# Optimization experiments

Measured on AMD Instinct MI355X. Metric: run time of the kernel, lower is better.

The kernel has to match this reference:

```python
import jax, jax.numpy as jnp
import numpy as np

EPS = 1e-5  # norm_eps


def setup_inputs() -> dict:
    key = jax.random.key(0)
    ks = jax.random.split(key, 9)
    N, C, T, H, W = 2, 1024, 8, 28, 28
    Di = 512
    s = 0.02  # weight init scale
    return {
        "x": jax.random.normal(ks[0], (N, C, T, H, W), jnp.float32),
        "w_theta": jax.random.normal(ks[1], (Di, C), jnp.float32) * s,
        "b_theta": jax.random.normal(ks[2], (Di,), jnp.float32) * s,
        "w_phi": jax.random.normal(ks[3], (Di, C), jnp.float32) * s,
        "b_phi": jax.random.normal(ks[4], (Di,), jnp.float32) * s,
        "w_g": jax.random.normal(ks[5], (Di, C), jnp.float32) * s,
        "b_g": jax.random.normal(ks[6], (Di,), jnp.float32) * s,
        "w_out": jax.random.normal(ks[7], (C, Di), jnp.float32) * s,
        "b_out": jax.random.normal(ks[8], (C,), jnp.float32) * s,
    }


def reference(x, w_theta, b_theta, w_phi, b_phi, w_g, b_g, w_out, b_out):
    # ProgressNL forward at step==0 (y == x), pool_size=None,
    # instantiation='softmax', norm_type='layernorm' (GroupNorm(1, C, affine=False)).
    N, C, T, H, W = x.shape
    Di = w_theta.shape[0]
    xf = x.reshape(N, C, T * H * W)  # flatten spatio-temporal tokens

    # 1x1x1 convs == per-token matmuls
    theta = jnp.einsum('dc,nct->ndt', w_theta, xf) + b_theta[None, :, None]  # [N,Di,THW]
    phi = jnp.einsum('dc,nct->ndt', w_phi, xf) + b_phi[None, :, None]
    g = jnp.einsum('dc,nct->ndt', w_g, xf) + b_g[None, :, None]

    # attention: softmax(theta^T phi / sqrt(Di)) @ g^T
    scores = jnp.einsum('nct,ncp->ntp', theta, phi) * (Di ** -0.5)  # [N,THW,THW]
    attn = jax.nn.softmax(scores, axis=-1)
    o = jnp.einsum('ntp,ncp->nct', attn, g)  # [N,Di,THW]

    # output 1x1x1 conv
    p = jnp.einsum('cd,ndt->nct', w_out, o) + b_out[None, :, None]  # [N,C,THW]

    # GroupNorm(1, C, affine=False): normalize over (C,T,H,W) per sample
    mean = jnp.mean(p, axis=(1, 2), keepdims=True)
    var = jnp.var(p, axis=(1, 2), keepdims=True)
    p = (p - mean) * jax.lax.rsqrt(var + EPS)

    return x + p.reshape(N, C, T, H, W)
```

## Files before the change

### kernel.cpp

```cpp
#include <hip/hip_runtime.h>

typedef _Float16 f16x8 __attribute__((ext_vector_type(8)));
typedef _Float16 f16x4 __attribute__((ext_vector_type(4)));
typedef float    f32x4 __attribute__((ext_vector_type(4)));

#define THW 6272
#define CCH 1024
#define DI  512

__device__ __forceinline__ void gload16(const _Float16* g, _Float16* l)
{
    __builtin_amdgcn_global_load_lds(
        (const __attribute__((address_space(1))) void*)g,
        (__attribute__((address_space(3))) void*)l, 16, 0, 0);
}

template<typename OUT_T, int BM, bool BIAS_M, bool BIAS_N, bool EXPP, bool GNP, bool RSC>
__global__ __launch_bounds__(256, 3)
void gemm_nt(const _Float16* __restrict__ A, size_t lda, size_t sAn,
             const _Float16* __restrict__ Bt, size_t ldb, size_t sBn,
             OUT_T* __restrict__ C, size_t ldc, size_t sCn,
             int K, int Kfull, float alpha,
             const float* __restrict__ bias_m,
             const float* __restrict__ bias_n,
             float* __restrict__ psum,
             const float* __restrict__ row_scale,
             int rows_ps,
             int gx, int gy)
{
    constexpr int MF = BM / 32;
    __shared__ _Float16 As[BM * 64];
    __shared__ _Float16 Bs[128 * 64];
    __shared__ float rs[4], rs2[4];
    const int tid  = threadIdx.x;
    const int lane = tid & 63;
    const int wave = tid >> 6;
    const int wr = wave >> 1, wc = wave & 1;

    const int nwg = gridDim.x;
    const int q = nwg >> 3, rr = nwg & 7;
    const int xcd = blockIdx.x & 7, seq = blockIdx.x >> 3;
    const int wg = (xcd < rr ? xcd * (q + 1) : rr * (q + 1) + (xcd - rr) * q) + seq;
    const int zz  = wg / (gx * gy);
    const int rem = wg - zz * gx * gy;
    const int by  = rem / gx, bx = rem - by * gx;
    const int n   = zz & 1;
    const int ks  = zz >> 1;

    const int koff = ks * K;
    const int klen = (Kfull - koff < K) ? (Kfull - koff) : K;

    A  += (size_t)n * sAn + (size_t)by * BM * lda + koff;
    Bt += (size_t)n * sBn + (size_t)bx * 128 * ldb + koff;

    const int srow = lane >> 3, sk = (lane & 7) * 8;
    const _Float16* gA = A  + (size_t)(wave * (MF * 8) + srow) * lda + sk;
    const _Float16* gB = Bt + (size_t)(wave * 32 + srow) * ldb + sk;
    _Float16* lA = As + wave * (MF * 512) + lane * 8;
    _Float16* lB = Bs + wave * 2048 + lane * 8;

    const int r  = lane & 15;
    const int kg = lane >> 4;

    f32x4 acc[MF][4] = {};

    for (int kt = 0; kt < klen; kt += 64) {
#pragma unroll
        for (int i = 0; i < MF; i++)
            gload16(gA + (size_t)(i * 8) * lda, lA + i * 512);
#pragma unroll
        for (int i = 0; i < 4; i++)
            gload16(gB + (size_t)(i * 8) * ldb, lB + i * 512);
        gA += 64; gB += 64;
        __syncthreads();
#pragma unroll
        for (int kk = 0; kk < 2; kk++) {
            f16x8 af[MF], bf[4];
#pragma unroll
            for (int mf = 0; mf < MF; mf++)
                af[mf] = *(const f16x8*)(As + (wr * (BM / 2) + mf * 16 + r) * 64 + kk * 32 + kg * 8);
#pragma unroll
            for (int nf = 0; nf < 4; nf++)
                bf[nf] = *(const f16x8*)(Bs + (wc * 64 + nf * 16 + r) * 64 + kk * 32 + kg * 8);
#pragma unroll
            for (int mf = 0; mf < MF; mf++)
#pragma unroll
                for (int nf = 0; nf < 4; nf++)
                    acc[mf][nf] = __builtin_amdgcn_mfma_f32_16x16x32_f16(
                        af[mf], bf[nf], acc[mf][nf], 0, 0, 0);
        }
        __syncthreads();
    }

    C += (size_t)zz * sCn;
    float gs = 0.f, gs2 = 0.f;
#pragma unroll
    for (int mf = 0; mf < MF; mf++) {
#pragma unroll
        for (int qi = 0; qi < 4; qi++) {
            size_t row = (size_t)by * BM + wr * (BM / 2) + mf * 16 + kg * 4 + qi;
            float bm = BIAS_M ? bias_m[row] : 0.f;
            float sc = RSC ? row_scale[(size_t)n * rows_ps + row] : 1.f;
            float rsum = 0.f;
#pragma unroll
            for (int nf = 0; nf < 4; nf++) {
                size_t col = (size_t)bx * 128 + wc * 64 + nf * 16 + r;
                float val = acc[mf][nf][qi] * alpha + bm + (BIAS_N ? bias_n[col] : 0.f);
                if (EXPP) {
                    float e = __expf(val);
                    rsum += e;
                    C[row * ldc + col] = (OUT_T)e;
                } else {
                    C[row * ldc + col] = (OUT_T)(RSC ? val * sc : val);
                }
                if (GNP) { gs += val; gs2 += val * val; }
            }
            if (EXPP) {
                rsum += __shfl_xor(rsum, 1);
                rsum += __shfl_xor(rsum, 2);
                rsum += __shfl_xor(rsum, 4);
                rsum += __shfl_xor(rsum, 8);
                if (r == 0)
                    psum[((size_t)n * rows_ps + row) * 98 + bx * 2 + wc] = rsum;
            }
        }
    }
    if (GNP) {
        for (int o = 32; o; o >>= 1) {
            gs  += __shfl_xor(gs, o);
            gs2 += __shfl_xor(gs2, o);
        }
        if (lane == 0) { rs[wave] = gs; rs2[wave] = gs2; }
        __syncthreads();
        if (tid == 0) {
            psum[(size_t)wg * 2]     = rs[0] + rs[1] + rs[2] + rs[3];
            psum[(size_t)wg * 2 + 1] = rs2[0] + rs2[1] + rs2[2] + rs2[3];
        }
    }
}

__global__ __launch_bounds__(256)
void rowsum_inv(const float* __restrict__ psum, float* __restrict__ inv, int nrows)
{
    int rI = blockIdx.x * 256 + threadIdx.x;
    if (rI < nrows) {
        const float* p = psum + (size_t)rI * 98;
        float s = 0.f;
#pragma unroll 7
        for (int i = 0; i < 98; i++) s += p[i];
        inv[rI] = 1.f / s;
    }
}

__global__ __launch_bounds__(256)
void combine4(const _Float16* __restrict__ Op, _Float16* __restrict__ Ot,
              int tr, int t0)
{
    const int per_n8 = tr * 64;
    int idx = blockIdx.x * 256 + threadIdx.x;
    if (idx >= 2 * per_n8) return;
    int n = idx / per_n8;
    int rem = idx - n * per_n8;
    int t = rem >> 6, d8 = rem & 63;
    const size_t slice = (size_t)tr * 512;
    float o[8] = {};
#pragma unroll
    for (int ks = 0; ks < 4; ks++) {
        f16x8 v = *(const f16x8*)(Op + (size_t)(ks * 2 + n) * slice + (size_t)rem * 8);
#pragma unroll
        for (int j = 0; j < 8; j++) o[j] += (float)v[j];
    }
    f16x8 w;
#pragma unroll
    for (int j = 0; j < 8; j++) w[j] = (_Float16)o[j];
    *(f16x8*)(Ot + ((size_t)(n * THW + t0 + t) * DI + d8 * 8)) = w;
}

__global__ __launch_bounds__(256)
void pack_weights(const float* __restrict__ wt, const float* __restrict__ wp,
                  const float* __restrict__ wg, const float* __restrict__ wo,
                  const float* __restrict__ bt, const float* __restrict__ bp,
                  _Float16* __restrict__ Wtp, _Float16* __restrict__ Wg,
                  _Float16* __restrict__ Wo, float* __restrict__ btp)
{
    int i = blockIdx.x * 256 + threadIdx.x;
    if (i < 512 * 1024) {
        Wtp[i]              = (_Float16)wt[i];
        Wtp[i + 512 * 1024] = (_Float16)wp[i];
        Wg[i]               = (_Float16)wg[i];
        Wo[i]               = (_Float16)wo[i];
    }
    if (i < 512) { btp[i] = bt[i]; btp[i + 512] = bp[i]; }
}

__global__ __launch_bounds__(256)
void transpose_cast(const float* __restrict__ x, _Float16* __restrict__ xT)
{
    __shared__ float tile[32][33];
    const int n  = blockIdx.z;
    const int t0 = blockIdx.x * 32;
    const int c0 = blockIdx.y * 32;
    const int tx = threadIdx.x & 31, ty = threadIdx.x >> 5;
    const float* xp = x + ((size_t)n * CCH + c0) * THW + t0;
#pragma unroll
    for (int i = 0; i < 4; i++) {
        int c = ty + i * 8;
        tile[c][tx] = xp[(size_t)c * THW + tx];
    }
    __syncthreads();
    _Float16* op = xT + ((size_t)n * THW + t0) * CCH + c0;
#pragma unroll
    for (int i = 0; i < 4; i++) {
        int t = ty + i * 8;
        op[(size_t)t * CCH + tx] = (_Float16)tile[tx][t];
    }
}

__global__ __launch_bounds__(256)
void reduce_final(const float* __restrict__ partials, float* __restrict__ stats, int nblk)
{
    const int n = blockIdx.x;
    float s = 0.f, s2 = 0.f;
    for (int i = threadIdx.x; i < nblk; i += 256) {
        s  += partials[((size_t)n * nblk + i) * 2];
        s2 += partials[((size_t)n * nblk + i) * 2 + 1];
    }
    for (int o = 32; o; o >>= 1) { s += __shfl_xor(s, o); s2 += __shfl_xor(s2, o); }
    __shared__ float rs[4], rs2[4];
    if ((threadIdx.x & 63) == 0) { rs[threadIdx.x >> 6] = s; rs2[threadIdx.x >> 6] = s2; }
    __syncthreads();
    if (threadIdx.x == 0) {
        float S1 = rs[0] + rs[1] + rs[2] + rs[3];
        float S2 = rs2[0] + rs2[1] + rs2[2] + rs2[3];
        const float invc = 1.f / ((float)CCH * (float)THW);
        float mean = S1 * invc;
        float var  = S2 * invc - mean * mean;
        stats[n * 2]     = mean;
        stats[n * 2 + 1] = rsqrtf(var + 1e-5f);
    }
}

__global__ __launch_bounds__(256)
void final_residual(const float* __restrict__ x, float* __restrict__ pc_out,
                    const float* __restrict__ stats, size_t total4)
{
    const size_t per_n4 = (size_t)CCH * THW / 4;
    for (size_t i = (size_t)blockIdx.x * 256 + threadIdx.x; i < total4;
         i += (size_t)gridDim.x * 256) {
        int n = (int)(i / per_n4);
        float mean = stats[n * 2], rstd = stats[n * 2 + 1];
        f32x4 xv = ((const f32x4*)x)[i];
        f32x4 pv = ((f32x4*)pc_out)[i];
        f32x4 ov;
#pragma unroll
        for (int j = 0; j < 4; j++) ov[j] = xv[j] + (pv[j] - mean) * rstd;
        ((f32x4*)pc_out)[i] = ov;
    }
}

extern "C" void kernel_launch(void* const* d_in, const int* in_sizes, int n_in,
                              void* d_out, int out_size, void* d_ws, size_t ws_size,
                              hipStream_t stream)
{
    const float* x  = (const float*)d_in[0];
    const float* wt = (const float*)d_in[1];
    const float* bt = (const float*)d_in[2];
    const float* wp = (const float*)d_in[3];
    const float* bp = (const float*)d_in[4];
    const float* wg = (const float*)d_in[5];
    const float* bg = (const float*)d_in[6];
    const float* wo = (const float*)d_in[7];
    const float* bo = (const float*)d_in[8];
    float* out = (float*)d_out;

    char* ws = (char*)d_ws;
    size_t off = 0;
    auto alloc = [&](size_t b) -> void* {
        off = (off + 255) & ~(size_t)255;
        void* p = ws + off;
        off += b;
        return p;
    };

    _Float16* Wtp = (_Float16*)alloc((size_t)1024 * 1024 * 2);
    _Float16* Wg  = (_Float16*)alloc((size_t)512 * 1024 * 2);
    _Float16* Wo  = (_Float16*)alloc((size_t)1024 * 512 * 2);
    float*    btp = (float*)alloc(1024 * 4);
    _Float16* xT  = (_Float16*)alloc((size_t)2 * THW * CCH * 2);
    _Float16* tpg = (_Float16*)alloc((size_t)2 * THW * 1024 * 2);
    _Float16* g   = (_Float16*)alloc((size_t)2 * DI * THW * 2);
    _Float16* Ot  = (_Float16*)alloc((size_t)2 * THW * DI * 2);
    float*    gnp   = (float*)alloc((size_t)784 * 2 * 4);
    float*    stats = (float*)alloc(4 * 4);

    const size_t tile_bytes = (size_t)2 * 128 * (THW * 2 + 98 * 4 + 4);
    size_t avail = (ws_size > off + 256) ? ws_size - off - 256 : 0;
    int tiles_fit = (int)(avail / tile_bytes);
    if (tiles_fit < 1) tiles_fit = 1;
    if (tiles_fit > 49) tiles_fit = 49;
    int nch = (49 + tiles_fit - 1) / tiles_fit;
    int tpc = (49 + nch - 1) / nch;

    _Float16* S    = (_Float16*)alloc((size_t)2 * tpc * 128 * THW * 2);
    float*    psum = (float*)alloc((size_t)2 * tpc * 128 * 98 * 4);
    float*    inv  = (float*)alloc((size_t)2 * tpc * 128 * 4);
    _Float16* Opart = (_Float16*)out;

    const size_t sXT = (size_t)THW * CCH;
    const size_t sG  = (size_t)DI * THW;

    pack_weights<<<2048, 256, 0, stream>>>(wt, wp, wg, wo, bt, bp, Wtp, Wg, Wo, btp);
    transpose_cast<<<dim3(THW / 32, CCH / 32, 2), 256, 0, stream>>>(x, xT);

    gemm_nt<_Float16, 128, false, true, false, false, false><<<8 * 49 * 2, 256, 0, stream>>>(
        xT, CCH, sXT, Wtp, CCH, 0, tpg, 1024, sXT, CCH, CCH, 1.f,
        nullptr, btp, nullptr, nullptr, 0, 8, 49);

    gemm_nt<_Float16, 64, true, false, false, false, false><<<49 * 8 * 2, 256, 0, stream>>>(
        Wg, CCH, 0, xT, CCH, sXT, g, THW, sG, CCH, CCH, 1.f,
        bg, nullptr, nullptr, nullptr, 0, 49, 8);

    const float scale = 0.044194173824159216f;
    for (int ch = 0; ch < nch; ch++) {
        int tile0 = ch * tpc;
        int tiles = (49 - tile0 < tpc) ? (49 - tile0) : tpc;
        size_t t0 = (size_t)tile0 * 128;
        int tchRows = tiles * 128;

        gemm_nt<_Float16, 128, false, false, true, false, false><<<49 * tiles * 2, 256, 0, stream>>>(
            tpg + t0 * 1024, 1024, sXT, tpg + 512, 1024, sXT,
            S, THW, (size_t)tchRows * THW, DI, DI, scale,
            nullptr, nullptr, psum, nullptr, tchRows, 49, tiles);

        rowsum_inv<<<(2 * tchRows + 255) / 256, 256, 0, stream>>>(psum, inv, 2 * tchRows);

        gemm_nt<_Float16, 128, false, false, false, false, true><<<4 * tiles * 8, 256, 0, stream>>>(
            S, THW, (size_t)tchRows * THW, g, THW, sG,
            Opart, DI, (size_t)tchRows * DI, 1600, THW, 1.f,
            nullptr, nullptr, nullptr, inv, tchRows, 4, tiles);

        combine4<<<(tchRows * 128 + 255) / 256, 256, 0, stream>>>(
            Opart, Ot, tchRows, (int)t0);
    }

    gemm_nt<float, 128, true, false, false, true, false><<<49 * 8 * 2, 256, 0, stream>>>(
        Wo, DI, 0, Ot, DI, sG, out, THW, (size_t)CCH * THW, DI, DI, 1.f,
        bo, nullptr, gnp, nullptr, 0, 49, 8);

    reduce_final<<<2, 256, 0, stream>>>(gnp, stats, 392);
    final_residual<<<2048, 256, 0, stream>>>(x, out, stats, (size_t)2 * CCH * THW / 4);
}
```

Before: 395.2 us.

## Transpose GEMM epilogue to write column-major with vectorized row stores

```diff
diff --git a/kernel.cpp b/kernel.cpp
--- a/kernel.cpp
+++ b/kernel.cpp
@@ -24,7 +24,7 @@
              const float* __restrict__ bias_m,
              const float* __restrict__ bias_n,
              float* __restrict__ psum,
-             const float* __restrict__ row_scale,
+             const float* __restrict__ col_scale,
              int rows_ps,
              int gx, int gy)
 {
@@ -94,35 +94,44 @@
 
     C += (size_t)zz * sCn;
     float gs = 0.f, gs2 = 0.f;
-#pragma unroll
-    for (int mf = 0; mf < MF; mf++) {
-#pragma unroll
-        for (int qi = 0; qi < 4; qi++) {
-            size_t row = (size_t)by * BM + wr * (BM / 2) + mf * 16 + kg * 4 + qi;
-            float bm = BIAS_M ? bias_m[row] : 0.f;
-            float sc = RSC ? row_scale[(size_t)n * rows_ps + row] : 1.f;
-            float rsum = 0.f;
-#pragma unroll
-            for (int nf = 0; nf < 4; nf++) {
-                size_t col = (size_t)bx * 128 + wc * 64 + nf * 16 + r;
-                float val = acc[mf][nf][qi] * alpha + bm + (BIAS_N ? bias_n[col] : 0.f);
-                if (EXPP) {
-                    float e = __expf(val);
-                    rsum += e;
-                    C[row * ldc + col] = (OUT_T)e;
-                } else {
-                    C[row * ldc + col] = (OUT_T)(RSC ? val * sc : val);
-                }
+    const size_t rowb0 = (size_t)by * BM + wr * (BM / 2) + kg * 4;
+
+#pragma unroll
+    for (int nf = 0; nf < 4; nf++) {
+        const size_t col = (size_t)bx * 128 + wc * 64 + nf * 16 + r;
+        const float bn = BIAS_N ? bias_n[col] : 0.f;
+        const float sc = RSC ? col_scale[(size_t)n * rows_ps + col] : 1.f;
+        float rsum = 0.f;
+        OUT_T* cp = C + col * ldc + rowb0;
+#pragma unroll
+        for (int mf = 0; mf < MF; mf++) {
+            f32x4 bm4 = {0.f, 0.f, 0.f, 0.f};
+            if (BIAS_M) bm4 = *(const f32x4*)(bias_m + rowb0 + mf * 16);
+            float v[4];
+#pragma unroll
+            for (int qi = 0; qi < 4; qi++) {
+                float val = acc[mf][nf][qi] * alpha + bm4[qi] + bn;
+                if (EXPP) { val = __expf(val); rsum += val; }
+                else if (RSC) val *= sc;
                 if (GNP) { gs += val; gs2 += val * val; }
+                v[qi] = val;
             }
-            if (EXPP) {
-                rsum += __shfl_xor(rsum, 1);
-                rsum += __shfl_xor(rsum, 2);
-                rsum += __shfl_xor(rsum, 4);
-                rsum += __shfl_xor(rsum, 8);
-                if (r == 0)
-                    psum[((size_t)n * rows_ps + row) * 98 + bx * 2 + wc] = rsum;
+            if constexpr (sizeof(OUT_T) == 2) {
+                f16x4 o;
+                o[0] = (_Float16)v[0]; o[1] = (_Float16)v[1];
+                o[2] = (_Float16)v[2]; o[3] = (_Float16)v[3];
+                *(f16x4*)(cp + mf * 16) = o;
+            } else {
+                f32x4 o;
+                o[0] = v[0]; o[1] = v[1]; o[2] = v[2]; o[3] = v[3];
+                *(f32x4*)(cp + mf * 16) = o;
             }
+        }
+        if (EXPP) {
+            rsum += __shfl_xor(rsum, 16);
+            rsum += __shfl_xor(rsum, 32);
+            if (kg == 0)
+                psum[((size_t)n * rows_ps + col) * 98 + by * 2 + wr] = rsum;
         }
     }
     if (GNP) {
@@ -312,13 +321,13 @@
     pack_weights<<<2048, 256, 0, stream>>>(wt, wp, wg, wo, bt, bp, Wtp, Wg, Wo, btp);
     transpose_cast<<<dim3(THW / 32, CCH / 32, 2), 256, 0, stream>>>(x, xT);
 
-    gemm_nt<_Float16, 128, false, true, false, false, false><<<8 * 49 * 2, 256, 0, stream>>>(
-        xT, CCH, sXT, Wtp, CCH, 0, tpg, 1024, sXT, CCH, CCH, 1.f,
-        nullptr, btp, nullptr, nullptr, 0, 8, 49);
-
-    gemm_nt<_Float16, 64, true, false, false, false, false><<<49 * 8 * 2, 256, 0, stream>>>(
-        Wg, CCH, 0, xT, CCH, sXT, g, THW, sG, CCH, CCH, 1.f,
-        bg, nullptr, nullptr, nullptr, 0, 49, 8);
+    gemm_nt<_Float16, 128, true, false, false, false, false><<<49 * 8 * 2, 256, 0, stream>>>(
+        Wtp, CCH, 0, xT, CCH, sXT, tpg, 1024, sXT, CCH, CCH, 1.f,
+        btp, nullptr, nullptr, nullptr, 0, 49, 8);
+
+    gemm_nt<_Float16, 64, false, true, false, false, false><<<4 * 98 * 2, 256, 0, stream>>>(
+        xT, CCH, sXT, Wg, CCH, 0, g, THW, sG, CCH, CCH, 1.f,
+        nullptr, bg, nullptr, nullptr, 0, 4, 98);
 
     const float scale = 0.044194173824159216f;
     for (int ch = 0; ch < nch; ch++) {
@@ -327,25 +336,25 @@
         size_t t0 = (size_t)tile0 * 128;
         int tchRows = tiles * 128;
 
-        gemm_nt<_Float16, 128, false, false, true, false, false><<<49 * tiles * 2, 256, 0, stream>>>(
-            tpg + t0 * 1024, 1024, sXT, tpg + 512, 1024, sXT,
+        gemm_nt<_Float16, 128, false, false, true, false, false><<<tiles * 49 * 2, 256, 0, stream>>>(
+            tpg + 512, 1024, sXT, tpg + t0 * 1024, 1024, sXT,
             S, THW, (size_t)tchRows * THW, DI, DI, scale,
-            nullptr, nullptr, psum, nullptr, tchRows, 49, tiles);
+            nullptr, nullptr, psum, nullptr, tchRows, tiles, 49);
 
         rowsum_inv<<<(2 * tchRows + 255) / 256, 256, 0, stream>>>(psum, inv, 2 * tchRows);
 
-        gemm_nt<_Float16, 128, false, false, false, false, true><<<4 * tiles * 8, 256, 0, stream>>>(
-            S, THW, (size_t)tchRows * THW, g, THW, sG,
+        gemm_nt<_Float16, 128, false, false, false, false, true><<<tiles * 4 * 8, 256, 0, stream>>>(
+            g, THW, sG, S, THW, (size_t)tchRows * THW,
             Opart, DI, (size_t)tchRows * DI, 1600, THW, 1.f,
-            nullptr, nullptr, nullptr, inv, tchRows, 4, tiles);
+            nullptr, nullptr, nullptr, inv, tchRows, tiles, 4);
 
         combine4<<<(tchRows * 128 + 255) / 256, 256, 0, stream>>>(
             Opart, Ot, tchRows, (int)t0);
     }
 
-    gemm_nt<float, 128, true, false, false, true, false><<<49 * 8 * 2, 256, 0, stream>>>(
-        Wo, DI, 0, Ot, DI, sG, out, THW, (size_t)CCH * THW, DI, DI, 1.f,
-        bo, nullptr, gnp, nullptr, 0, 49, 8);
+    gemm_nt<float, 128, false, true, false, true, false><<<8 * 49 * 2, 256, 0, stream>>>(
+        Ot, DI, sG, Wo, DI, 0, out, THW, (size_t)CCH * THW, DI, DI, 1.f,
+        nullptr, bo, gnp, nullptr, 0, 8, 49);
 
     reduce_final<<<2, 256, 0, stream>>>(gnp, stats, 392);
     final_residual<<<2048, 256, 0, stream>>>(x, out, stats, (size_t)2 * CCH * THW / 4);
```

After: 425.7 us. 7.7% more time.
